# Kernel tuning notes

Hardware: AMD Instinct MI355X
Metric: run time of the kernel (lower is better)

Reference implementation:

```python
import jax, jax.numpy as jnp
import numpy as np

B, E, D, O = 2048, 64, 512, 512  # batch, n_options, latent_dim, out_dim


def setup_inputs() -> dict:
    key = jax.random.key(0)
    k1, k2, k3, k4 = jax.random.split(key, 4)
    bound = 1.0 / np.sqrt(D)  # kaiming/fan_in-style scale
    x = jax.random.normal(k1, (B, D), dtype=jnp.float32)
    option = jax.random.randint(k2, (B,), 0, E, dtype=jnp.int32)
    weight = jax.random.uniform(k3, (E, D, O), dtype=jnp.float32, minval=-bound, maxval=bound)
    bias = jax.random.uniform(k4, (E, O), dtype=jnp.float32, minval=-bound, maxval=bound)
    return {"x": x, "option": option, "weight": weight, "bias": bias}


def reference(x, option, weight, bias):
    # out[b] = x[b] @ weight[option[b]] + bias[option[b]]
    w_g = jnp.take(weight, option, axis=0)          # [B, D, O] per-sample gathered weights
    b_g = jnp.take(bias, option, axis=0)            # [B, O]
    out = jnp.einsum('bd,bdo->bo', x, w_g) + b_g    # [B, O]
    return out
```

## Files before the change

kernel.cpp:

```cpp
#include <hip/hip_runtime.h>

#define B_N 2048
#define E_N 64
#define D_N 512
#define O_N 512
#define ON  64
#define MC  64
#define NT  16

typedef __bf16 bf16x8 __attribute__((ext_vector_type(8)));
typedef float  f32x4  __attribute__((ext_vector_type(4)));

__device__ __forceinline__ unsigned short f2bf(float f) {
  unsigned int u = __float_as_uint(f);
  u = (u + 0x7FFFu + ((u >> 16) & 1u)) >> 16;
  return (unsigned short)u;
}

__global__ __launch_bounds__(256)
void bucket_kernel(const int* __restrict__ opt, int* __restrict__ cnt,
                   int* __restrict__ list) {
  int b = blockIdx.x * 256 + threadIdx.x;
  int e = opt[b];
  int slot = atomicAdd(&cnt[e], 1);
  list[e * B_N + slot] = b;
}

__device__ __forceinline__ void step_compute(
    const unsigned short* __restrict__ xs, const float* __restrict__ wsp,
    int kt, int g, int col64, int r0, int r1, f32x4& acc0, f32x4& acc1) {
  const int kb = kt * 32 + g * 8;
  const int key = (r0 & 7) << 3;
  union { uint4 u; bf16x8 v; } a0, a1;
  a0.u = *reinterpret_cast<const uint4*>(&xs[r0 * 512 + ((kb ^ key))]);
  a1.u = *reinterpret_cast<const uint4*>(&xs[r1 * 512 + ((kb ^ key))]);
  union { unsigned short us[8]; bf16x8 v; } bf_;
  const int csw = col64 ^ (g << 4);
#pragma unroll
  for (int j = 0; j < 8; ++j) bf_.us[j] = f2bf(wsp[(g * 8 + j) * 64 + csw]);
  acc0 = __builtin_amdgcn_mfma_f32_16x16x32_bf16(a0.v, bf_.v, acc0, 0, 0, 0);
  acc1 = __builtin_amdgcn_mfma_f32_16x16x32_bf16(a1.v, bf_.v, acc1, 0, 0, 0);
}

#define DMA_W(KT, WSBUF) do {                                                  \
    const float* _src = wexp + (size_t)((KT) * 32 + dk) * O_N + o0 + scol;     \
    __builtin_amdgcn_global_load_lds(                                          \
        (const __attribute__((address_space(1))) void*)_src,                   \
        (__attribute__((address_space(3))) void*)&WSBUF[wave * 256], 16, 0, 0);\
  } while (0)

#define WAIT1_BAR() asm volatile("s_waitcnt vmcnt(1)\ns_barrier" ::: "memory")
#define WAIT0_BAR() asm volatile("s_waitcnt vmcnt(0)\ns_barrier" ::: "memory")
#define LGKM_BAR()  asm volatile("s_waitcnt lgkmcnt(0)\ns_barrier" ::: "memory")

__global__ __launch_bounds__(512)
void gemm_kernel(const float* __restrict__ x, const float* __restrict__ w,
                 const float* __restrict__ bias, const int* __restrict__ cnt,
                 const int* __restrict__ list, float* __restrict__ out) {
  __shared__ unsigned short xs[MC * 512];
  __shared__ float wsA[32 * 64];
  __shared__ float wsB[32 * 64];

  const int e    = blockIdx.x;
  const int o0   = blockIdx.y * ON;
  const int t    = threadIdx.x;
  const int lane = t & 63;
  const int wave = t >> 6;
  const int wc   = wave & 3;
  const int wg   = wave >> 2;
  const int n    = cnt[e];
  if (n == 0) return;

  const float* wexp = w + (size_t)e * D_N * O_N;
  const int m_in  = lane & 15;
  const int g     = lane >> 4;
  const int col64 = wc * 16 + m_in;
  const float bval = bias[e * O_N + o0 + col64];
  const int* mylist = list + e * B_N;
  const int r0 = wg * 32 + m_in;
  const int r1 = r0 + 16;

  const int dk   = 4 * wave + (lane >> 4);
  const int skey = ((dk >> 3) & 3) << 4;
  const int scol = ((lane & 15) * 4) ^ skey;

  for (int m0 = 0; m0 < n; m0 += MC) {
    __syncthreads();
    DMA_W(0, wsA);
#pragma unroll
    for (int i = 0; i < 16; ++i) {
      int idx = t + i * 512;
      int row = idx >> 7;
      int c4  = idx & 127;
      int s   = m0 + row;
      ushort4 v = make_ushort4(0, 0, 0, 0);
      if (s < n) {
        const float4 xv = *reinterpret_cast<const float4*>(x + (size_t)mylist[s] * D_N + c4 * 4);
        v = make_ushort4(f2bf(xv.x), f2bf(xv.y), f2bf(xv.z), f2bf(xv.w));
      }
      *reinterpret_cast<ushort4*>(&xs[row * 512 + ((c4 * 4) ^ ((row & 7) << 3))]) = v;
    }
    __syncthreads();

    f32x4 acc0 = {0.f, 0.f, 0.f, 0.f};
    f32x4 acc1 = {0.f, 0.f, 0.f, 0.f};

#pragma unroll 1
    for (int kt = 0; kt < NT; kt += 2) {
      DMA_W(kt + 1, wsB);
      WAIT1_BAR();
      step_compute(xs, wsA, kt, g, col64, r0, r1, acc0, acc1);
      LGKM_BAR();
      if (kt + 2 < NT) { DMA_W(kt + 2, wsA); WAIT1_BAR(); }
      else             { WAIT0_BAR(); }
      step_compute(xs, wsB, kt + 1, g, col64, r0, r1, acc0, acc1);
      LGKM_BAR();
    }

#pragma unroll
    for (int r = 0; r < 4; ++r) {
      int sl = wg * 32 + g * 4 + r;
      int s  = m0 + sl;
      if (s < n)  out[(size_t)mylist[s]  * O_N + o0 + col64] = acc0[r] + bval;
      int s2 = m0 + sl + 16;
      if (s2 < n) out[(size_t)mylist[s2] * O_N + o0 + col64] = acc1[r] + bval;
    }
  }
}

extern "C" void kernel_launch(void* const* d_in, const int* in_sizes, int n_in,
                              void* d_out, int out_size, void* d_ws, size_t ws_size,
                              hipStream_t stream) {
  const float* x      = (const float*)d_in[0];
  const int*   option = (const int*)d_in[1];
  const float* weight = (const float*)d_in[2];
  const float* bias   = (const float*)d_in[3];
  float* out = (float*)d_out;

  int* cnt  = (int*)d_ws;
  int* list = (int*)((char*)d_ws + 256);

  hipMemsetAsync(cnt, 0, E_N * sizeof(int), stream);
  bucket_kernel<<<B_N / 256, 256, 0, stream>>>(option, cnt, list);
  gemm_kernel<<<dim3(E_N, O_N / ON), 512, 0, stream>>>(x, weight, bias, cnt, list, out);
}
```

Measured before the change: 33.18 us.

## Deepen weight prefetch to a four-stage ring and halve the row chunk

Replaces the two-buffer weight staging with a four-slot LDS ring that keeps three tile DMAs in flight ahead of compute. It also halves the row chunk per expert from 64 to 32, so each wave computes one MFMA tile instead of two and less LDS is needed for x. The aim is to hide global-load latency on the weight stream and cut padded work for experts with few rows. The cost is that experts with more than 32 rows now loop twice and re-stream their weight slice. The prefetch also issues wasted wrap-around tile loads at the end of each chunk.

```diff
diff --git a/kernel.cpp b/kernel.cpp
--- a/kernel.cpp
+++ b/kernel.cpp
@@ -4,8 +4,7 @@
 #define E_N 64
 #define D_N 512
 #define O_N 512
-#define ON  64
-#define MC  64
+#define MC  32
 #define NT  16
 
 typedef __bf16 bf16x8 __attribute__((ext_vector_type(8)));
@@ -26,43 +25,15 @@
   list[e * B_N + slot] = b;
 }
 
-__device__ __forceinline__ void step_compute(
-    const unsigned short* __restrict__ xs, const float* __restrict__ wsp,
-    int kt, int g, int col64, int r0, int r1, f32x4& acc0, f32x4& acc1) {
-  const int kb = kt * 32 + g * 8;
-  const int key = (r0 & 7) << 3;
-  union { uint4 u; bf16x8 v; } a0, a1;
-  a0.u = *reinterpret_cast<const uint4*>(&xs[r0 * 512 + ((kb ^ key))]);
-  a1.u = *reinterpret_cast<const uint4*>(&xs[r1 * 512 + ((kb ^ key))]);
-  union { unsigned short us[8]; bf16x8 v; } bf_;
-  const int csw = col64 ^ (g << 4);
-#pragma unroll
-  for (int j = 0; j < 8; ++j) bf_.us[j] = f2bf(wsp[(g * 8 + j) * 64 + csw]);
-  acc0 = __builtin_amdgcn_mfma_f32_16x16x32_bf16(a0.v, bf_.v, acc0, 0, 0, 0);
-  acc1 = __builtin_amdgcn_mfma_f32_16x16x32_bf16(a1.v, bf_.v, acc1, 0, 0, 0);
-}
-
-#define DMA_W(KT, WSBUF) do {                                                  \
-    const float* _src = wexp + (size_t)((KT) * 32 + dk) * O_N + o0 + scol;     \
-    __builtin_amdgcn_global_load_lds(                                          \
-        (const __attribute__((address_space(1))) void*)_src,                   \
-        (__attribute__((address_space(3))) void*)&WSBUF[wave * 256], 16, 0, 0);\
-  } while (0)
-
-#define WAIT1_BAR() asm volatile("s_waitcnt vmcnt(1)\ns_barrier" ::: "memory")
-#define WAIT0_BAR() asm volatile("s_waitcnt vmcnt(0)\ns_barrier" ::: "memory")
-#define LGKM_BAR()  asm volatile("s_waitcnt lgkmcnt(0)\ns_barrier" ::: "memory")
-
 __global__ __launch_bounds__(512)
 void gemm_kernel(const float* __restrict__ x, const float* __restrict__ w,
                  const float* __restrict__ bias, const int* __restrict__ cnt,
                  const int* __restrict__ list, float* __restrict__ out) {
   __shared__ unsigned short xs[MC * 512];
-  __shared__ float wsA[32 * 64];
-  __shared__ float wsB[32 * 64];
+  __shared__ float ws[4][32 * 64];
 
   const int e    = blockIdx.x;
-  const int o0   = blockIdx.y * ON;
+  const int o0   = blockIdx.y * 64;
   const int t    = threadIdx.x;
   const int lane = t & 63;
   const int wave = t >> 6;
@@ -77,18 +48,38 @@
   const int col64 = wc * 16 + m_in;
   const float bval = bias[e * O_N + o0 + col64];
   const int* mylist = list + e * B_N;
-  const int r0 = wg * 32 + m_in;
-  const int r1 = r0 + 16;
+  const int r0   = wg * 16 + m_in;
+  const int akey = (r0 & 7) << 3;
+  const int csw  = col64 ^ (g << 4);
 
   const int dk   = 4 * wave + (lane >> 4);
   const int skey = ((dk >> 3) & 3) << 4;
   const int scol = ((lane & 15) * 4) ^ skey;
 
+#define DMA_T(TT) do {                                                         \
+    const float* _src =                                                        \
+        wexp + (size_t)(((TT) & 15) * 32 + dk) * O_N + o0 + scol;              \
+    __builtin_amdgcn_global_load_lds(                                          \
+        (const __attribute__((address_space(1))) void*)_src,                   \
+        (__attribute__((address_space(3))) void*)&ws[(TT) & 3][wave * 256],    \
+        16, 0, 0);                                                             \
+  } while (0)
+
+#define COMPUTE(KT) do {                                                       \
+    const float* wsp = &ws[(KT) & 3][0];                                       \
+    const int kk = ((KT) * 32 + g * 8) ^ akey;                                 \
+    union { uint4 u; bf16x8 v; } a0;                                           \
+    a0.u = *reinterpret_cast<const uint4*>(&xs[r0 * 512 + kk]);                \
+    union { unsigned short us[8]; bf16x8 v; } bw;                              \
+    _Pragma("unroll")                                                          \
+    for (int j = 0; j < 8; ++j) bw.us[j] = f2bf(wsp[(g * 8 + j) * 64 + csw]);  \
+    acc0 = __builtin_amdgcn_mfma_f32_16x16x32_bf16(a0.v, bw.v, acc0, 0, 0, 0); \
+  } while (0)
+
   for (int m0 = 0; m0 < n; m0 += MC) {
     __syncthreads();
-    DMA_W(0, wsA);
 #pragma unroll
-    for (int i = 0; i < 16; ++i) {
+    for (int i = 0; i < 8; ++i) {
       int idx = t + i * 512;
       int row = idx >> 7;
       int c4  = idx & 127;
@@ -103,29 +94,26 @@
     __syncthreads();
 
     f32x4 acc0 = {0.f, 0.f, 0.f, 0.f};
-    f32x4 acc1 = {0.f, 0.f, 0.f, 0.f};
 
+    DMA_T(0); DMA_T(1); DMA_T(2);
 #pragma unroll 1
-    for (int kt = 0; kt < NT; kt += 2) {
-      DMA_W(kt + 1, wsB);
-      WAIT1_BAR();
-      step_compute(xs, wsA, kt, g, col64, r0, r1, acc0, acc1);
-      LGKM_BAR();
-      if (kt + 2 < NT) { DMA_W(kt + 2, wsA); WAIT1_BAR(); }
-      else             { WAIT0_BAR(); }
-      step_compute(xs, wsB, kt + 1, g, col64, r0, r1, acc0, acc1);
-      LGKM_BAR();
+    for (int kt = 0; kt < NT; ++kt) {
+      DMA_T(kt + 3);
+      asm volatile("s_waitcnt vmcnt(3)\ns_barrier" ::: "memory");
+      COMPUTE(kt);
+      asm volatile("s_waitcnt lgkmcnt(0)\ns_barrier" ::: "memory");
     }
 
 #pragma unroll
     for (int r = 0; r < 4; ++r) {
-      int sl = wg * 32 + g * 4 + r;
+      int sl = wg * 16 + g * 4 + r;
       int s  = m0 + sl;
-      if (s < n)  out[(size_t)mylist[s]  * O_N + o0 + col64] = acc0[r] + bval;
-      int s2 = m0 + sl + 16;
-      if (s2 < n) out[(size_t)mylist[s2] * O_N + o0 + col64] = acc1[r] + bval;
+      if (s < n) out[(size_t)mylist[s] * O_N + o0 + col64] = acc0[r] + bval;
     }
   }
+  asm volatile("s_waitcnt vmcnt(0)" ::: "memory");
+#undef DMA_T
+#undef COMPUTE
 }
 
 extern "C" void kernel_launch(void* const* d_in, const int* in_sizes, int n_in,
@@ -142,5 +130,5 @@
 
   hipMemsetAsync(cnt, 0, E_N * sizeof(int), stream);
   bucket_kernel<<<B_N / 256, 256, 0, stream>>>(option, cnt, list);
-  gemm_kernel<<<dim3(E_N, O_N / ON), 512, 0, stream>>>(x, weight, bias, cnt, list, out);
+  gemm_kernel<<<dim3(E_N, O_N / 64), 512, 0, stream>>>(x, weight, bias, cnt, list, out);
 }
```

After: 43.43 us. +30.9%, slower.
